# Optimization experiments

Measured on AMD Instinct MI355X. Metric: run time of the kernel, lower is better.

## Reference

```python
import jax, jax.numpy as jnp
import numpy as np

L = 2          # lags
D = 16         # latent_size (number of per-channel MLPs)
H = 64         # hidden_dim
SLOPE = 0.2    # LeakyReLU negative slope used by NLayerLeakyMLP


def _forward(x, W0, b0, W1, b1, W2, b2, Wout, bout):
    B, T, _ = x.shape
    nwin = T - L
    # sliding windows of size L+1 along time: [B, nwin, L+1, D]
    idx = jnp.arange(nwin)[:, None] + jnp.arange(L + 1)[None, :]
    w = x[:, idx]
    N = B * nwin
    yy = w[:, :, :L, :].reshape(N, L * D)   # past L steps, flattened
    xx = w[:, :, L, :].reshape(N, D)        # current step, per channel
    # per-channel MLP inputs, stacked over channels: [D, N, L*D+1]
    inputs = jnp.concatenate(
        [jnp.broadcast_to(yy[None], (D, N, L * D)), xx.T[:, :, None]], axis=-1)

    def mlp(inp):  # all D channel-MLPs at once
        h = jax.nn.leaky_relu(jnp.einsum('dni,dhi->dnh', inp, W0) + b0[:, None, :], SLOPE)
        h = jax.nn.leaky_relu(jnp.einsum('dnh,dkh->dnk', h, W1) + b1[:, None, :], SLOPE)
        h = jax.nn.leaky_relu(jnp.einsum('dnh,dkh->dnk', h, W2) + b2[:, None, :], SLOPE)
        return jnp.einsum('dnh,doh->dno', h, Wout) + bout[:, None, :]  # [D, N, 1]

    # d g_i(inputs)/d (last coord) via one forward-mode JVP (replaces the
    # full batched Jacobian + diagonal extraction of the torch version)
    tangent = jnp.zeros_like(inputs).at[..., -1].set(1.0)
    out, dout = jax.jvp(mlp, (inputs,), (tangent,))
    residuals = out[:, :, 0].T.reshape(B, nwin, D)
    logabsdet = jnp.log(jnp.abs(dout[:, :, 0])).sum(0)          # sum over channels -> [N]
    sum_log_abs_det = logabsdet.reshape(B, nwin).sum(1)          # [B]
    return residuals, sum_log_abs_det


def setup_inputs():
    key = jax.random.key(0)
    ks = jax.random.split(key, 9)
    B, T = 32, 512
    in_f = L * D + 1
    s = 0.1
    return {
        "x": jax.random.normal(ks[0], (B, T, D), jnp.float32),
        "W0": jax.random.normal(ks[1], (D, H, in_f), jnp.float32) * s,
        "b0": jax.random.normal(ks[2], (D, H), jnp.float32) * s,
        "W1": jax.random.normal(ks[3], (D, H, H), jnp.float32) * s,
        "b1": jax.random.normal(ks[4], (D, H), jnp.float32) * s,
        "W2": jax.random.normal(ks[5], (D, H, H), jnp.float32) * s,
        "b2": jax.random.normal(ks[6], (D, H), jnp.float32) * s,
        "Wout": jax.random.normal(ks[7], (D, 1, H), jnp.float32) * s,
        "bout": jax.random.normal(ks[8], (D, 1), jnp.float32) * s,
    }


def reference(x, W0, b0, W1, b1, W2, b2, Wout, bout):
    return _forward(x, W0, b0, W1, b1, W2, b2, Wout, bout)
```

## Files before the change

### kernel.cpp

```cpp
#include <hip/hip_runtime.h>
#include <hip/hip_bf16.h>
#include <math.h>

#define NB 32
#define SEQT 512
#define DDIM 16
#define NWIN 510
#define NTOT (NB*NWIN)
#define SLOPE 0.2f
#define NI 3
#define GW 192
#define NGR 85
#define NGP 88

typedef __attribute__((ext_vector_type(8))) short sh8;
typedef __attribute__((ext_vector_type(4))) float f4;

#define W0B_OFF 0
#define W1B_OFF 65536
#define W2B_OFF 196608
#define WCOL_OFF 327680
#define RED_OFF 331776
#define NPREP 164864

static __device__ __forceinline__ unsigned short bfb(float f){
    union { __hip_bfloat16 h; unsigned short u; } cv;
    cv.h = __float2bfloat16(f);
    return cv.u;
}
static __device__ __forceinline__ unsigned pk2(float a, float b){
    return (unsigned)bfb(a) | ((unsigned)bfb(b) << 16);
}

__global__ void prep(const float* __restrict__ W0, const float* __restrict__ W1,
                     const float* __restrict__ W2, unsigned char* __restrict__ wsb){
    int e = blockIdx.x*256 + threadIdx.x;
    if (e < 32768){
        unsigned short* W0b = (unsigned short*)(wsb + W0B_OFF);
        int d = e >> 11, r = e & 2047, h = r >> 5, k = r & 31;
        W0b[e] = bfb(W0[(d*64 + h)*33 + k]);
    } else if (e < 98304){
        ((unsigned short*)(wsb + W1B_OFF))[e - 32768] = bfb(W1[e - 32768]);
    } else if (e < 163840){
        ((unsigned short*)(wsb + W2B_OFF))[e - 98304] = bfb(W2[e - 98304]);
    } else if (e < NPREP){
        int i = e - 163840;
        int d = i >> 6, h = i & 63;
        ((float*)(wsb + WCOL_OFF))[i] = W0[(d*64 + h)*33 + 32];
    }
}

__global__ __launch_bounds__(256, 3) void mlp(
    const float* __restrict__ x,
    const float* __restrict__ bias0, const float* __restrict__ bias1,
    const float* __restrict__ bias2,
    const float* __restrict__ Wout, const float* __restrict__ boutp,
    const unsigned char* __restrict__ wsb,
    float* __restrict__ red, float* __restrict__ out)
{
    __shared__ __align__(16) unsigned char bufA[GW*128];
    __shared__ __align__(16) unsigned char bufB[GW*128];

    const int tid  = threadIdx.x;
    const int lane = tid & 63;
    const int w    = tid >> 6;
    const int nl   = lane & 15;
    const int hi   = lane >> 4;
    const int rsw  = (nl & 7) << 4;

    const int bid = blockIdx.x;
    const int d   = (bid >> 3) & 15;
    const int g   = ((bid >> 7) << 3) | (bid & 7);
    if (g >= NGR) return;

    const unsigned char* W0b = wsb + W0B_OFF + d*4096;
    const unsigned char* W1b = wsb + W1B_OFF + d*8192;
    const unsigned char* W2b = wsb + W2B_OFF + d*8192;

    int   bb[NI];
    float xxv[NI];
    union { uint4 u; sh8 s; } in[NI];
    #pragma unroll
    for (int i=0;i<NI;++i){
        int n = g*GW + 48*w + nl + 16*i;
        int b = n / NWIN, t = n - b*NWIN;
        bb[i] = b;
        const float* gp = x + (size_t)(b*SEQT + t)*DDIM + 8*hi;
        float4 p0 = ((const float4*)gp)[0];
        float4 p1 = ((const float4*)gp)[1];
        in[i].u.x = pk2(p0.x,p0.y); in[i].u.y = pk2(p0.z,p0.w);
        in[i].u.z = pk2(p1.x,p1.y); in[i].u.w = pk2(p1.z,p1.w);
        xxv[i] = x[(size_t)(b*SEQT + t + 2)*DDIM + d];
    }

    f4 aA[NI][4], aB[NI][4];

    #pragma unroll
    for (int t=0;t<4;++t){
        float4 bv = *(const float4*)(bias0 + d*64 + 16*t + 4*hi);
        #pragma unroll
        for (int i=0;i<NI;++i) aA[i][t] = (f4){bv.x,bv.y,bv.z,bv.w};
    }
    __builtin_amdgcn_s_setprio(1);
    #pragma unroll
    for (int t=0;t<4;++t){
        sh8 af = *(const sh8*)&W0b[((16*t+nl)*32 + 8*hi)*2];
        #pragma unroll
        for (int i=0;i<NI;++i)
            aA[i][t] = __builtin_amdgcn_mfma_f32_16x16x32_bf16(af, in[i].s, aA[i][t], 0,0,0);
    }
    __builtin_amdgcn_s_setprio(0);

    {
        const float* wcolp = (const float*)(wsb + WCOL_OFF) + d*64;
        #pragma unroll
        for (int t=0;t<4;++t){
            float4 wv = *(const float4*)(wcolp + 16*t + 4*hi);
            float wc[4] = {wv.x, wv.y, wv.z, wv.w};
            #pragma unroll
            for (int i=0;i<NI;++i){
                const int row = 48*w + nl + 16*i;
                float v[4], tv[4];
                #pragma unroll
                for (int r=0;r<4;++r){
                    float a = fmaf(wc[r], xxv[i], aA[i][t][r]);
                    v[r]  = fmaxf(a, SLOPE*a);
                    tv[r] = (a >= 0.f) ? wc[r] : SLOPE*wc[r];
                }
                uint2 ph; ph.x = pk2(v[0],v[1]);  ph.y = pk2(v[2],v[3]);
                *(uint2*)&bufA[row*128 + ((32*t + 8*hi) ^ rsw)] = ph;
                uint2 pt; pt.x = pk2(tv[0],tv[1]); pt.y = pk2(tv[2],tv[3]);
                *(uint2*)&bufB[row*128 + ((32*t + 8*hi) ^ rsw)] = pt;
            }
        }
    }

    #pragma unroll
    for (int t=0;t<4;++t){
        float4 bv = *(const float4*)(bias1 + d*64 + 16*t + 4*hi);
        #pragma unroll
        for (int i=0;i<NI;++i){
            aA[i][t] = (f4){bv.x,bv.y,bv.z,bv.w};
            aB[i][t] = (f4){0.f,0.f,0.f,0.f};
        }
    }
    __builtin_amdgcn_s_setprio(1);
    #pragma unroll
    for (int ks=0; ks<2; ++ks){
        sh8 fA[NI], fB[NI];
        #pragma unroll
        for (int i=0;i<NI;++i){
            const int row = 48*w + nl + 16*i;
            fA[i] = *(const sh8*)&bufA[row*128 + ((64*ks + 16*hi) ^ rsw)];
            fB[i] = *(const sh8*)&bufB[row*128 + ((64*ks + 16*hi) ^ rsw)];
        }
        #pragma unroll
        for (int t=0;t<4;++t){
            sh8 af = *(const sh8*)&W1b[((16*t+nl)*64 + 32*ks + 8*hi)*2];
            #pragma unroll
            for (int i=0;i<NI;++i){
                aA[i][t] = __builtin_amdgcn_mfma_f32_16x16x32_bf16(af, fA[i], aA[i][t], 0,0,0);
                aB[i][t] = __builtin_amdgcn_mfma_f32_16x16x32_bf16(af, fB[i], aB[i][t], 0,0,0);
            }
        }
    }
    __builtin_amdgcn_s_setprio(0);
    #pragma unroll
    for (int i=0;i<NI;++i){
        const int row = 48*w + nl + 16*i;
        #pragma unroll
        for (int t=0;t<4;++t){
            float v[4], tv[4];
            #pragma unroll
            for (int r=0;r<4;++r){
                float a = aA[i][t][r];
                v[r] = fmaxf(a, SLOPE*a);
                float q = aB[i][t][r];
                tv[r] = (a >= 0.f) ? q : SLOPE*q;
            }
            uint2 ph; ph.x = pk2(v[0],v[1]); ph.y = pk2(v[2],v[3]);
            *(uint2*)&bufA[row*128 + ((32*t + 8*hi) ^ rsw)] = ph;
            uint2 pt; pt.x = pk2(tv[0],tv[1]); pt.y = pk2(tv[2],tv[3]);
            *(uint2*)&bufB[row*128 + ((32*t + 8*hi) ^ rsw)] = pt;
        }
    }

    #pragma unroll
    for (int t=0;t<4;++t){
        float4 bv = *(const float4*)(bias2 + d*64 + 16*t + 4*hi);
        #pragma unroll
        for (int i=0;i<NI;++i){
            aA[i][t] = (f4){bv.x,bv.y,bv.z,bv.w};
            aB[i][t] = (f4){0.f,0.f,0.f,0.f};
        }
    }
    __builtin_amdgcn_s_setprio(1);
    #pragma unroll
    for (int ks=0; ks<2; ++ks){
        sh8 fA[NI], fB[NI];
        #pragma unroll
        for (int i=0;i<NI;++i){
            const int row = 48*w + nl + 16*i;
            fA[i] = *(const sh8*)&bufA[row*128 + ((64*ks + 16*hi) ^ rsw)];
            fB[i] = *(const sh8*)&bufB[row*128 + ((64*ks + 16*hi) ^ rsw)];
        }
        #pragma unroll
        for (int t=0;t<4;++t){
            sh8 af = *(const sh8*)&W2b[((16*t+nl)*64 + 32*ks + 8*hi)*2];
            #pragma unroll
            for (int i=0;i<NI;++i){
                aA[i][t] = __builtin_amdgcn_mfma_f32_16x16x32_bf16(af, fA[i], aA[i][t], 0,0,0);
                aB[i][t] = __builtin_amdgcn_mfma_f32_16x16x32_bf16(af, fB[i], aB[i][t], 0,0,0);
            }
        }
    }
    __builtin_amdgcn_s_setprio(0);

    float res[NI], dres[NI];
    #pragma unroll
    for (int i=0;i<NI;++i){ res[i] = 0.f; dres[i] = 0.f; }
    #pragma unroll
    for (int t=0;t<4;++t){
        float4 ov = *(const float4*)(Wout + d*64 + 16*t + 4*hi);
        float wo[4] = {ov.x, ov.y, ov.z, ov.w};
        #pragma unroll
        for (int i=0;i<NI;++i){
            #pragma unroll
            for (int r=0;r<4;++r){
                float a  = aA[i][t][r];
                float h3 = fmaxf(a, SLOPE*a);
                res[i] = fmaf(wo[r], h3, res[i]);
                float q  = aB[i][t][r];
                float tv = (a >= 0.f) ? q : SLOPE*q;
                dres[i] = fmaf(wo[r], tv, dres[i]);
            }
        }
    }
    const float bo = boutp[d];
    float la[NI];
    #pragma unroll
    for (int i=0;i<NI;++i){
        res[i]  += __shfl_xor(res[i], 16);  res[i]  += __shfl_xor(res[i], 32);
        dres[i] += __shfl_xor(dres[i], 16); dres[i] += __shfl_xor(dres[i], 32);
        la[i] = __logf(fabsf(dres[i]));
    }
    if (hi == 0){
        #pragma unroll
        for (int i=0;i<NI;++i){
            int n = g*GW + 48*w + nl + 16*i;
            out[(size_t)n*DDIM + d] = res[i] + bo;
        }
    }

    {
        int cb0 = (g*GW) / NWIN;
        float v0 = 0.f, v1 = 0.f;
        #pragma unroll
        for (int i=0;i<NI;++i){
            v0 += (bb[i] == cb0    ) ? la[i] : 0.f;
            v1 += (bb[i] == cb0 + 1) ? la[i] : 0.f;
        }
        #pragma unroll
        for (int s = 1; s < 16; s <<= 1){
            v0 += __shfl_xor(v0, s);
            v1 += __shfl_xor(v1, s);
        }
        if (lane == 0){
            red[((size_t)(g*4 + w)*16 + d)*2 + 0] = v0;
            red[((size_t)(g*4 + w)*16 + d)*2 + 1] = v1;
        }
    }
}

__global__ void final_red(const float* __restrict__ red, float* __restrict__ sld){
    __shared__ float pp[DDIM][16];
    const int b = blockIdx.x;
    const int tid = threadIdx.x;
    const int d = tid & 15, j = tid >> 4;
    float s = 0.f;
    for (int gw = j; gw < NGR*4; gw += 16){
        int g = gw >> 2;
        int cb0 = (g*GW)/NWIN;
        const float* r = red + ((size_t)gw*16 + d)*2;
        if (cb0     == b) s += r[0];
        if (cb0 + 1 == b) s += r[1];
    }
    pp[d][j] = s;
    __syncthreads();
    if (tid < DDIM){
        float a = 0.f;
        #pragma unroll
        for (int k=0;k<16;++k) a += pp[tid][k];
        pp[tid][0] = a;
    }
    __syncthreads();
    if (tid == 0){
        float a = 0.f;
        #pragma unroll
        for (int dd=0; dd<DDIM; ++dd) a += pp[dd][0];
        sld[b] = a;
    }
}

extern "C" void kernel_launch(void* const* d_in, const int* in_sizes, int n_in,
                              void* d_out, int out_size, void* d_ws, size_t ws_size,
                              hipStream_t stream) {
    const float* x    = (const float*)d_in[0];
    const float* W0   = (const float*)d_in[1];
    const float* b0   = (const float*)d_in[2];
    const float* W1   = (const float*)d_in[3];
    const float* b1   = (const float*)d_in[4];
    const float* W2   = (const float*)d_in[5];
    const float* b2   = (const float*)d_in[6];
    const float* Wout = (const float*)d_in[7];
    const float* bout = (const float*)d_in[8];
    float* out = (float*)d_out;
    unsigned char* wsb = (unsigned char*)d_ws;

    prep<<<(NPREP + 255)/256, 256, 0, stream>>>(W0, W1, W2, wsb);

    mlp<<<NGP*DDIM, 256, 0, stream>>>(x, b0, b1, b2, Wout, bout, wsb,
                                      (float*)(wsb + RED_OFF), out);

    final_red<<<NB, 256, 0, stream>>>((const float*)(wsb + RED_OFF),
                                      out + (size_t)NTOT*DDIM);
}
```

Measured before the change: 42.81 us.

## Split primal and tangent MFMA passes, packing sign masks into bitfields

Instead of keeping separate accumulators for the primal and tangent (JVP) paths live at the same time, each hidden layer now runs two sequential MFMA passes through one accumulator array. The LeakyReLU sign of each primal pre-activation is stored as bits in two 32-bit masks and applied to the tangent pass afterwards. This roughly halves accumulator register pressure, and launch bounds are raised from 3 to 4 blocks per SIMD to use the freed registers. The cost is less instruction-level overlap between the two MFMA chains, extra serialization between the passes, and some bit-manipulation work.

```diff
diff --git a/kernel.cpp b/kernel.cpp
--- a/kernel.cpp
+++ b/kernel.cpp
@@ -50,7 +50,7 @@
     }
 }
 
-__global__ __launch_bounds__(256, 3) void mlp(
+__global__ __launch_bounds__(256, 4) void mlp(
     const float* __restrict__ x,
     const float* __restrict__ bias0, const float* __restrict__ bias1,
     const float* __restrict__ bias2,
@@ -93,13 +93,13 @@
         xxv[i] = x[(size_t)(b*SEQT + t + 2)*DDIM + d];
     }
 
-    f4 aA[NI][4], aB[NI][4];
+    f4 acc[NI][4];
 
     #pragma unroll
     for (int t=0;t<4;++t){
         float4 bv = *(const float4*)(bias0 + d*64 + 16*t + 4*hi);
         #pragma unroll
-        for (int i=0;i<NI;++i) aA[i][t] = (f4){bv.x,bv.y,bv.z,bv.w};
+        for (int i=0;i<NI;++i) acc[i][t] = (f4){bv.x,bv.y,bv.z,bv.w};
     }
     __builtin_amdgcn_s_setprio(1);
     #pragma unroll
@@ -107,7 +107,7 @@
         sh8 af = *(const sh8*)&W0b[((16*t+nl)*32 + 8*hi)*2];
         #pragma unroll
         for (int i=0;i<NI;++i)
-            aA[i][t] = __builtin_amdgcn_mfma_f32_16x16x32_bf16(af, in[i].s, aA[i][t], 0,0,0);
+            acc[i][t] = __builtin_amdgcn_mfma_f32_16x16x32_bf16(af, in[i].s, acc[i][t], 0,0,0);
     }
     __builtin_amdgcn_s_setprio(0);
 
@@ -123,7 +123,7 @@
                 float v[4], tv[4];
                 #pragma unroll
                 for (int r=0;r<4;++r){
-                    float a = fmaf(wc[r], xxv[i], aA[i][t][r]);
+                    float a = fmaf(wc[r], xxv[i], acc[i][t][r]);
                     v[r]  = fmaxf(a, SLOPE*a);
                     tv[r] = (a >= 0.f) ? wc[r] : SLOPE*wc[r];
                 }
@@ -135,33 +135,27 @@
         }
     }
 
+    unsigned m2lo = 0, m2hi = 0;
+
     #pragma unroll
     for (int t=0;t<4;++t){
         float4 bv = *(const float4*)(bias1 + d*64 + 16*t + 4*hi);
         #pragma unroll
-        for (int i=0;i<NI;++i){
-            aA[i][t] = (f4){bv.x,bv.y,bv.z,bv.w};
-            aB[i][t] = (f4){0.f,0.f,0.f,0.f};
-        }
+        for (int i=0;i<NI;++i) acc[i][t] = (f4){bv.x,bv.y,bv.z,bv.w};
     }
     __builtin_amdgcn_s_setprio(1);
     #pragma unroll
     for (int ks=0; ks<2; ++ks){
-        sh8 fA[NI], fB[NI];
-        #pragma unroll
-        for (int i=0;i<NI;++i){
-            const int row = 48*w + nl + 16*i;
-            fA[i] = *(const sh8*)&bufA[row*128 + ((64*ks + 16*hi) ^ rsw)];
-            fB[i] = *(const sh8*)&bufB[row*128 + ((64*ks + 16*hi) ^ rsw)];
-        }
+        sh8 fA[NI];
+        #pragma unroll
+        for (int i=0;i<NI;++i)
+            fA[i] = *(const sh8*)&bufA[(48*w + nl + 16*i)*128 + ((64*ks + 16*hi) ^ rsw)];
         #pragma unroll
         for (int t=0;t<4;++t){
             sh8 af = *(const sh8*)&W1b[((16*t+nl)*64 + 32*ks + 8*hi)*2];
             #pragma unroll
-            for (int i=0;i<NI;++i){
-                aA[i][t] = __builtin_amdgcn_mfma_f32_16x16x32_bf16(af, fA[i], aA[i][t], 0,0,0);
-                aB[i][t] = __builtin_amdgcn_mfma_f32_16x16x32_bf16(af, fB[i], aB[i][t], 0,0,0);
-            }
+            for (int i=0;i<NI;++i)
+                acc[i][t] = __builtin_amdgcn_mfma_f32_16x16x32_bf16(af, fA[i], acc[i][t], 0,0,0);
         }
     }
     __builtin_amdgcn_s_setprio(0);
@@ -170,55 +164,83 @@
         const int row = 48*w + nl + 16*i;
         #pragma unroll
         for (int t=0;t<4;++t){
-            float v[4], tv[4];
+            float v[4];
             #pragma unroll
             for (int r=0;r<4;++r){
-                float a = aA[i][t][r];
+                float a = acc[i][t][r];
+                unsigned neg = __float_as_uint(a) >> 31;
+                if (i < 2) m2lo |= neg << (i*16 + t*4 + r);
+                else       m2hi |= neg << (t*4 + r);
                 v[r] = fmaxf(a, SLOPE*a);
-                float q = aB[i][t][r];
-                tv[r] = (a >= 0.f) ? q : SLOPE*q;
             }
             uint2 ph; ph.x = pk2(v[0],v[1]); ph.y = pk2(v[2],v[3]);
             *(uint2*)&bufA[row*128 + ((32*t + 8*hi) ^ rsw)] = ph;
+        }
+    }
+
+    #pragma unroll
+    for (int t=0;t<4;++t)
+        #pragma unroll
+        for (int i=0;i<NI;++i) acc[i][t] = (f4){0.f,0.f,0.f,0.f};
+    __builtin_amdgcn_s_setprio(1);
+    #pragma unroll
+    for (int ks=0; ks<2; ++ks){
+        sh8 fB[NI];
+        #pragma unroll
+        for (int i=0;i<NI;++i)
+            fB[i] = *(const sh8*)&bufB[(48*w + nl + 16*i)*128 + ((64*ks + 16*hi) ^ rsw)];
+        #pragma unroll
+        for (int t=0;t<4;++t){
+            sh8 af = *(const sh8*)&W1b[((16*t+nl)*64 + 32*ks + 8*hi)*2];
+            #pragma unroll
+            for (int i=0;i<NI;++i)
+                acc[i][t] = __builtin_amdgcn_mfma_f32_16x16x32_bf16(af, fB[i], acc[i][t], 0,0,0);
+        }
+    }
+    __builtin_amdgcn_s_setprio(0);
+    #pragma unroll
+    for (int i=0;i<NI;++i){
+        const int row = 48*w + nl + 16*i;
+        #pragma unroll
+        for (int t=0;t<4;++t){
+            float tv[4];
+            #pragma unroll
+            for (int r=0;r<4;++r){
+                float q = acc[i][t][r];
+                unsigned neg = (i < 2) ? ((m2lo >> (i*16 + t*4 + r)) & 1u)
+                                       : ((m2hi >> (t*4 + r)) & 1u);
+                tv[r] = neg ? SLOPE*q : q;
+            }
             uint2 pt; pt.x = pk2(tv[0],tv[1]); pt.y = pk2(tv[2],tv[3]);
             *(uint2*)&bufB[row*128 + ((32*t + 8*hi) ^ rsw)] = pt;
         }
     }
 
+    unsigned m3lo = 0, m3hi = 0;
+    float res[NI] = {0.f, 0.f, 0.f};
+
     #pragma unroll
     for (int t=0;t<4;++t){
         float4 bv = *(const float4*)(bias2 + d*64 + 16*t + 4*hi);
         #pragma unroll
-        for (int i=0;i<NI;++i){
-            aA[i][t] = (f4){bv.x,bv.y,bv.z,bv.w};
-            aB[i][t] = (f4){0.f,0.f,0.f,0.f};
-        }
+        for (int i=0;i<NI;++i) acc[i][t] = (f4){bv.x,bv.y,bv.z,bv.w};
     }
     __builtin_amdgcn_s_setprio(1);
     #pragma unroll
     for (int ks=0; ks<2; ++ks){
-        sh8 fA[NI], fB[NI];
-        #pragma unroll
-        for (int i=0;i<NI;++i){
-            const int row = 48*w + nl + 16*i;
-            fA[i] = *(const sh8*)&bufA[row*128 + ((64*ks + 16*hi) ^ rsw)];
-            fB[i] = *(const sh8*)&bufB[row*128 + ((64*ks + 16*hi) ^ rsw)];
-        }
+        sh8 fA[NI];
+        #pragma unroll
+        for (int i=0;i<NI;++i)
+            fA[i] = *(const sh8*)&bufA[(48*w + nl + 16*i)*128 + ((64*ks + 16*hi) ^ rsw)];
         #pragma unroll
         for (int t=0;t<4;++t){
             sh8 af = *(const sh8*)&W2b[((16*t+nl)*64 + 32*ks + 8*hi)*2];
             #pragma unroll
-            for (int i=0;i<NI;++i){
-                aA[i][t] = __builtin_amdgcn_mfma_f32_16x16x32_bf16(af, fA[i], aA[i][t], 0,0,0);
-                aB[i][t] = __builtin_amdgcn_mfma_f32_16x16x32_bf16(af, fB[i], aB[i][t], 0,0,0);
-            }
-        }
-    }
-    __builtin_amdgcn_s_setprio(0);
-
-    float res[NI], dres[NI];
-    #pragma unroll
-    for (int i=0;i<NI;++i){ res[i] = 0.f; dres[i] = 0.f; }
+            for (int i=0;i<NI;++i)
+                acc[i][t] = __builtin_amdgcn_mfma_f32_16x16x32_bf16(af, fA[i], acc[i][t], 0,0,0);
+        }
+    }
+    __builtin_amdgcn_s_setprio(0);
     #pragma unroll
     for (int t=0;t<4;++t){
         float4 ov = *(const float4*)(Wout + d*64 + 16*t + 4*hi);
@@ -227,11 +249,50 @@
         for (int i=0;i<NI;++i){
             #pragma unroll
             for (int r=0;r<4;++r){
-                float a  = aA[i][t][r];
+                float a = acc[i][t][r];
+                unsigned neg = __float_as_uint(a) >> 31;
+                if (i < 2) m3lo |= neg << (i*16 + t*4 + r);
+                else       m3hi |= neg << (t*4 + r);
                 float h3 = fmaxf(a, SLOPE*a);
                 res[i] = fmaf(wo[r], h3, res[i]);
-                float q  = aB[i][t][r];
-                float tv = (a >= 0.f) ? q : SLOPE*q;
+            }
+        }
+    }
+
+    #pragma unroll
+    for (int t=0;t<4;++t)
+        #pragma unroll
+        for (int i=0;i<NI;++i) acc[i][t] = (f4){0.f,0.f,0.f,0.f};
+    __builtin_amdgcn_s_setprio(1);
+    #pragma unroll
+    for (int ks=0; ks<2; ++ks){
+        sh8 fB[NI];
+        #pragma unroll
+        for (int i=0;i<NI;++i)
+            fB[i] = *(const sh8*)&bufB[(48*w + nl + 16*i)*128 + ((64*ks + 16*hi) ^ rsw)];
+        #pragma unroll
+        for (int t=0;t<4;++t){
+            sh8 af = *(const sh8*)&W2b[((16*t+nl)*64 + 32*ks + 8*hi)*2];
+            #pragma unroll
+            for (int i=0;i<NI;++i)
+                acc[i][t] = __builtin_amdgcn_mfma_f32_16x16x32_bf16(af, fB[i], acc[i][t], 0,0,0);
+        }
+    }
+    __builtin_amdgcn_s_setprio(0);
+
+    float dres[NI] = {0.f, 0.f, 0.f};
+    #pragma unroll
+    for (int t=0;t<4;++t){
+        float4 ov = *(const float4*)(Wout + d*64 + 16*t + 4*hi);
+        float wo[4] = {ov.x, ov.y, ov.z, ov.w};
+        #pragma unroll
+        for (int i=0;i<NI;++i){
+            #pragma unroll
+            for (int r=0;r<4;++r){
+                float q = acc[i][t][r];
+                unsigned neg = (i < 2) ? ((m3lo >> (i*16 + t*4 + r)) & 1u)
+                                       : ((m3hi >> (t*4 + r)) & 1u);
+                float tv = neg ? SLOPE*q : q;
                 dres[i] = fmaf(wo[r], tv, dres[i]);
             }
         }
```

Measured after the change: 52.32 us. +22.2%, slower.

## Replace LDS activation staging with register cross-lane shuffles and shrink tiles

Applied to the files above, without the earlier changes.

The MFMA output fragments of each layer are kept in registers. They are rearranged into the next layer's B-operand layout with __shfl cross-lane exchanges, which removes the shared-memory buffers and their write/read round-trips. The group width drops from 192 to 128 rows (NI 3→2), giving 128 groups per channel, and a validity mask guards the tail rows. The shuffles add ds_bpermute traffic and VALU selects, and the grid has more blocks with less work each.

```diff
diff --git a/kernel.cpp b/kernel.cpp
--- a/kernel.cpp
+++ b/kernel.cpp
@@ -8,10 +8,9 @@
 #define NWIN 510
 #define NTOT (NB*NWIN)
 #define SLOPE 0.2f
-#define NI 3
-#define GW 192
-#define NGR 85
-#define NGP 88
+#define NI 2
+#define GW 128
+#define NG 128
 
 typedef __attribute__((ext_vector_type(8))) short sh8;
 typedef __attribute__((ext_vector_type(4))) float f4;
@@ -30,6 +29,21 @@
 }
 static __device__ __forceinline__ unsigned pk2(float a, float b){
     return (unsigned)bfb(a) | ((unsigned)bfb(b) << 16);
+}
+static __device__ __forceinline__ sh8 mk8(int w0, int w1, int w2, int w3){
+    union { uint4 u; sh8 s; } r;
+    r.u.x = (unsigned)w0; r.u.y = (unsigned)w1;
+    r.u.z = (unsigned)w2; r.u.w = (unsigned)w3;
+    return r.s;
+}
+static __device__ __forceinline__ sh8 xfrag(const uint2 pk[4], int ks,
+                                            int srcA, int srcB, int hs){
+    int a0x = __shfl((int)pk[2*ks  ].x, srcA), a0y = __shfl((int)pk[2*ks  ].y, srcA);
+    int a1x = __shfl((int)pk[2*ks+1].x, srcA), a1y = __shfl((int)pk[2*ks+1].y, srcA);
+    int b0x = __shfl((int)pk[2*ks  ].x, srcB), b0y = __shfl((int)pk[2*ks  ].y, srcB);
+    int b1x = __shfl((int)pk[2*ks+1].x, srcB), b1y = __shfl((int)pk[2*ks+1].y, srcB);
+    return mk8(hs ? a1x : a0x, hs ? a1y : a0y,
+               hs ? b1x : b0x, hs ? b1y : b0y);
 }
 
 __global__ void prep(const float* __restrict__ W0, const float* __restrict__ W1,
@@ -58,32 +72,33 @@
     const unsigned char* __restrict__ wsb,
     float* __restrict__ red, float* __restrict__ out)
 {
-    __shared__ __align__(16) unsigned char bufA[GW*128];
-    __shared__ __align__(16) unsigned char bufB[GW*128];
-
     const int tid  = threadIdx.x;
     const int lane = tid & 63;
     const int w    = tid >> 6;
     const int nl   = lane & 15;
     const int hi   = lane >> 4;
-    const int rsw  = (nl & 7) << 4;
+    const int hs   = hi >> 1;
+    const int srcA = nl + ((hi & 1) << 5);
+    const int srcB = srcA + 16;
 
     const int bid = blockIdx.x;
     const int d   = (bid >> 3) & 15;
     const int g   = ((bid >> 7) << 3) | (bid & 7);
-    if (g >= NGR) return;
 
     const unsigned char* W0b = wsb + W0B_OFF + d*4096;
     const unsigned char* W1b = wsb + W1B_OFF + d*8192;
     const unsigned char* W2b = wsb + W2B_OFF + d*8192;
 
     int   bb[NI];
+    bool  val[NI];
     float xxv[NI];
     union { uint4 u; sh8 s; } in[NI];
     #pragma unroll
     for (int i=0;i<NI;++i){
-        int n = g*GW + 48*w + nl + 16*i;
-        int b = n / NWIN, t = n - b*NWIN;
+        int n = g*GW + 32*w + 16*i + nl;
+        val[i] = (n < NTOT);
+        int ne = val[i] ? n : (NTOT-1);
+        int b = ne / NWIN, t = ne - b*NWIN;
         bb[i] = b;
         const float* gp = x + (size_t)(b*SEQT + t)*DDIM + 8*hi;
         float4 p0 = ((const float4*)gp)[0];
@@ -93,13 +108,14 @@
         xxv[i] = x[(size_t)(b*SEQT + t + 2)*DDIM + d];
     }
 
-    f4 aA[NI][4], aB[NI][4];
+    f4 accA[NI][4], accB[NI][4];
+    uint2 ph[NI][4], pt[NI][4];
 
     #pragma unroll
     for (int t=0;t<4;++t){
         float4 bv = *(const float4*)(bias0 + d*64 + 16*t + 4*hi);
         #pragma unroll
-        for (int i=0;i<NI;++i) aA[i][t] = (f4){bv.x,bv.y,bv.z,bv.w};
+        for (int i=0;i<NI;++i) accA[i][t] = (f4){bv.x,bv.y,bv.z,bv.w};
     }
     __builtin_amdgcn_s_setprio(1);
     #pragma unroll
@@ -107,7 +123,7 @@
         sh8 af = *(const sh8*)&W0b[((16*t+nl)*32 + 8*hi)*2];
         #pragma unroll
         for (int i=0;i<NI;++i)
-            aA[i][t] = __builtin_amdgcn_mfma_f32_16x16x32_bf16(af, in[i].s, aA[i][t], 0,0,0);
+            accA[i][t] = __builtin_amdgcn_mfma_f32_16x16x32_bf16(af, in[i].s, accA[i][t], 0,0,0);
     }
     __builtin_amdgcn_s_setprio(0);
 
@@ -119,18 +135,15 @@
             float wc[4] = {wv.x, wv.y, wv.z, wv.w};
             #pragma unroll
             for (int i=0;i<NI;++i){
-                const int row = 48*w + nl + 16*i;
                 float v[4], tv[4];
                 #pragma unroll
                 for (int r=0;r<4;++r){
-                    float a = fmaf(wc[r], xxv[i], aA[i][t][r]);
+                    float a = fmaf(wc[r], xxv[i], accA[i][t][r]);
                     v[r]  = fmaxf(a, SLOPE*a);
                     tv[r] = (a >= 0.f) ? wc[r] : SLOPE*wc[r];
                 }
-                uint2 ph; ph.x = pk2(v[0],v[1]);  ph.y = pk2(v[2],v[3]);
-                *(uint2*)&bufA[row*128 + ((32*t + 8*hi) ^ rsw)] = ph;
-                uint2 pt; pt.x = pk2(tv[0],tv[1]); pt.y = pk2(tv[2],tv[3]);
-                *(uint2*)&bufB[row*128 + ((32*t + 8*hi) ^ rsw)] = pt;
+                ph[i][t].x = pk2(v[0],v[1]);  ph[i][t].y = pk2(v[2],v[3]);
+                pt[i][t].x = pk2(tv[0],tv[1]); pt[i][t].y = pk2(tv[2],tv[3]);
             }
         }
     }
@@ -140,48 +153,45 @@
         float4 bv = *(const float4*)(bias1 + d*64 + 16*t + 4*hi);
         #pragma unroll
         for (int i=0;i<NI;++i){
-            aA[i][t] = (f4){bv.x,bv.y,bv.z,bv.w};
-            aB[i][t] = (f4){0.f,0.f,0.f,0.f};
-        }
-    }
-    __builtin_amdgcn_s_setprio(1);
+            accA[i][t] = (f4){bv.x,bv.y,bv.z,bv.w};
+            accB[i][t] = (f4){0.f,0.f,0.f,0.f};
+        }
+    }
     #pragma unroll
     for (int ks=0; ks<2; ++ks){
-        sh8 fA[NI], fB[NI];
-        #pragma unroll
-        for (int i=0;i<NI;++i){
-            const int row = 48*w + nl + 16*i;
-            fA[i] = *(const sh8*)&bufA[row*128 + ((64*ks + 16*hi) ^ rsw)];
-            fB[i] = *(const sh8*)&bufB[row*128 + ((64*ks + 16*hi) ^ rsw)];
-        }
+        sh8 fh[NI], ft[NI];
+        #pragma unroll
+        for (int i=0;i<NI;++i){
+            fh[i] = xfrag(ph[i], ks, srcA, srcB, hs);
+            ft[i] = xfrag(pt[i], ks, srcA, srcB, hs);
+        }
+        __builtin_amdgcn_s_setprio(1);
         #pragma unroll
         for (int t=0;t<4;++t){
             sh8 af = *(const sh8*)&W1b[((16*t+nl)*64 + 32*ks + 8*hi)*2];
             #pragma unroll
             for (int i=0;i<NI;++i){
-                aA[i][t] = __builtin_amdgcn_mfma_f32_16x16x32_bf16(af, fA[i], aA[i][t], 0,0,0);
-                aB[i][t] = __builtin_amdgcn_mfma_f32_16x16x32_bf16(af, fB[i], aB[i][t], 0,0,0);
-            }
-        }
-    }
-    __builtin_amdgcn_s_setprio(0);
+                accA[i][t] = __builtin_amdgcn_mfma_f32_16x16x32_bf16(af, fh[i], accA[i][t], 0,0,0);
+                accB[i][t] = __builtin_amdgcn_mfma_f32_16x16x32_bf16(af, ft[i], accB[i][t], 0,0,0);
+            }
+        }
+        __builtin_amdgcn_s_setprio(0);
+    }
+
     #pragma unroll
     for (int i=0;i<NI;++i){
-        const int row = 48*w + nl + 16*i;
         #pragma unroll
         for (int t=0;t<4;++t){
             float v[4], tv[4];
             #pragma unroll
             for (int r=0;r<4;++r){
-                float a = aA[i][t][r];
+                float a = accA[i][t][r];
                 v[r] = fmaxf(a, SLOPE*a);
-                float q = aB[i][t][r];
+                float q = accB[i][t][r];
                 tv[r] = (a >= 0.f) ? q : SLOPE*q;
             }
-            uint2 ph; ph.x = pk2(v[0],v[1]); ph.y = pk2(v[2],v[3]);
-            *(uint2*)&bufA[row*128 + ((32*t + 8*hi) ^ rsw)] = ph;
-            uint2 pt; pt.x = pk2(tv[0],tv[1]); pt.y = pk2(tv[2],tv[3]);
-            *(uint2*)&bufB[row*128 + ((32*t + 8*hi) ^ rsw)] = pt;
+            ph[i][t].x = pk2(v[0],v[1]);  ph[i][t].y = pk2(v[2],v[3]);
+            pt[i][t].x = pk2(tv[0],tv[1]); pt[i][t].y = pk2(tv[2],tv[3]);
         }
     }
 
@@ -190,31 +200,30 @@
         float4 bv = *(const float4*)(bias2 + d*64 + 16*t + 4*hi);
         #pragma unroll
         for (int i=0;i<NI;++i){
-            aA[i][t] = (f4){bv.x,bv.y,bv.z,bv.w};
-            aB[i][t] = (f4){0.f,0.f,0.f,0.f};
-        }
-    }
-    __builtin_amdgcn_s_setprio(1);
+            accA[i][t] = (f4){bv.x,bv.y,bv.z,bv.w};
+            accB[i][t] = (f4){0.f,0.f,0.f,0.f};
+        }
+    }
     #pragma unroll
     for (int ks=0; ks<2; ++ks){
-        sh8 fA[NI], fB[NI];
-        #pragma unroll
-        for (int i=0;i<NI;++i){
-            const int row = 48*w + nl + 16*i;
-            fA[i] = *(const sh8*)&bufA[row*128 + ((64*ks + 16*hi) ^ rsw)];
-            fB[i] = *(const sh8*)&bufB[row*128 + ((64*ks + 16*hi) ^ rsw)];
-        }
+        sh8 fh[NI], ft[NI];
+        #pragma unroll
+        for (int i=0;i<NI;++i){
+            fh[i] = xfrag(ph[i], ks, srcA, srcB, hs);
+            ft[i] = xfrag(pt[i], ks, srcA, srcB, hs);
+        }
+        __builtin_amdgcn_s_setprio(1);
         #pragma unroll
         for (int t=0;t<4;++t){
             sh8 af = *(const sh8*)&W2b[((16*t+nl)*64 + 32*ks + 8*hi)*2];
             #pragma unroll
             for (int i=0;i<NI;++i){
-                aA[i][t] = __builtin_amdgcn_mfma_f32_16x16x32_bf16(af, fA[i], aA[i][t], 0,0,0);
-                aB[i][t] = __builtin_amdgcn_mfma_f32_16x16x32_bf16(af, fB[i], aB[i][t], 0,0,0);
-            }
-        }
-    }
-    __builtin_amdgcn_s_setprio(0);
+                accA[i][t] = __builtin_amdgcn_mfma_f32_16x16x32_bf16(af, fh[i], accA[i][t], 0,0,0);
+                accB[i][t] = __builtin_amdgcn_mfma_f32_16x16x32_bf16(af, ft[i], accB[i][t], 0,0,0);
+            }
+        }
+        __builtin_amdgcn_s_setprio(0);
+    }
 
     float res[NI], dres[NI];
     #pragma unroll
@@ -227,10 +236,10 @@
         for (int i=0;i<NI;++i){
             #pragma unroll
             for (int r=0;r<4;++r){
-                float a  = aA[i][t][r];
+                float a  = accA[i][t][r];
                 float h3 = fmaxf(a, SLOPE*a);
                 res[i] = fmaf(wo[r], h3, res[i]);
-                float q  = aB[i][t][r];
+                float q  = accB[i][t][r];
                 float tv = (a >= 0.f) ? q : SLOPE*q;
                 dres[i] = fmaf(wo[r], tv, dres[i]);
             }
@@ -247,8 +256,10 @@
     if (hi == 0){
         #pragma unroll
         for (int i=0;i<NI;++i){
-            int n = g*GW + 48*w + nl + 16*i;
-            out[(size_t)n*DDIM + d] = res[i] + bo;
+            if (val[i]){
+                int n = g*GW + 32*w + 16*i + nl;
+                out[(size_t)n*DDIM + d] = res[i] + bo;
+            }
         }
     }
 
@@ -257,8 +268,10 @@
         float v0 = 0.f, v1 = 0.f;
         #pragma unroll
         for (int i=0;i<NI;++i){
-            v0 += (bb[i] == cb0    ) ? la[i] : 0.f;
-            v1 += (bb[i] == cb0 + 1) ? la[i] : 0.f;
+            if (val[i]){
+                v0 += (bb[i] == cb0    ) ? la[i] : 0.f;
+                v1 += (bb[i] == cb0 + 1) ? la[i] : 0.f;
+            }
         }
         #pragma unroll
         for (int s = 1; s < 16; s <<= 1){
@@ -278,7 +291,7 @@
     const int tid = threadIdx.x;
     const int d = tid & 15, j = tid >> 4;
     float s = 0.f;
-    for (int gw = j; gw < NGR*4; gw += 16){
+    for (int gw = j; gw < NG*4; gw += 16){
         int g = gw >> 2;
         int cb0 = (g*GW)/NWIN;
         const float* r = red + ((size_t)gw*16 + d)*2;
@@ -319,8 +332,8 @@
 
     prep<<<(NPREP + 255)/256, 256, 0, stream>>>(W0, W1, W2, wsb);
 
-    mlp<<<NGP*DDIM, 256, 0, stream>>>(x, b0, b1, b2, Wout, bout, wsb,
-                                      (float*)(wsb + RED_OFF), out);
+    mlp<<<NG*DDIM, 256, 0, stream>>>(x, b0, b1, b2, Wout, bout, wsb,
+                                     (float*)(wsb + RED_OFF), out);
 
     final_red<<<NB, 256, 0, stream>>>((const float*)(wsb + RED_OFF),
                                       out + (size_t)NTOT*DDIM);
```

Measured after the change: 45.73 us. 6.8% more time.
